# Optimization experiments

Measured on AMD Instinct MI355X. Metric: run time of the kernel, lower is better.

The kernel has to match this reference:

```python
import jax, jax.numpy as jnp
import numpy as np

N_HEAD = 16
D_MODEL = 1024
D_HEAD = 64
B = 2
S = 2048      # query length
M = 512       # memory length
K = S + M     # key length
L = 2 * K - 1 # relative position table length
SCALE = 1.0 / np.sqrt(D_MODEL)  # NOTE: module scales by 1/sqrt(d_model), not d_head
EPS = 1e-5


def layer_norm(x, gamma, beta):
    mu = jnp.mean(x, axis=-1, keepdims=True)
    var = jnp.mean(jnp.square(x - mu), axis=-1, keepdims=True)
    return (x - mu) * jax.lax.rsqrt(var + EPS) * gamma + beta


def skew(qpos, mem_len):
    # qpos: (B, H, S, 2K-1) -> relative-position scores aligned to keys (B, H, S, K)
    b, h, s, l = qpos.shape
    k_len = (l + 1) // 2
    pad = jnp.full((b, h, s, 1), -jnp.inf, dtype=qpos.dtype)
    rel = jnp.concatenate([qpos, pad], axis=-1)          # (B,H,S,2K)
    rel = rel.reshape(b, h, s * (l + 1))[..., : s * l]    # drop tail, shift rows
    rel = rel.reshape(b, h, s, l)
    start = (k_len - 1) - mem_len
    return rel[..., start : start + k_len]


def setup_inputs() -> dict:
    key = jax.random.key(0)
    ks = jax.random.split(key, 8)
    w_scale = 1.0 / np.sqrt(D_MODEL)
    hidden = jax.random.normal(ks[0], (B, S, D_MODEL), jnp.float32)
    memory = jax.random.normal(ks[1], (B, M, D_MODEL), jnp.float32)
    pos_emb = jax.random.normal(ks[2], (B, L, D_HEAD), jnp.float32)
    Wq = jax.random.normal(ks[3], (D_MODEL, N_HEAD * D_HEAD), jnp.float32) * w_scale
    Wk = jax.random.normal(ks[4], (D_MODEL, N_HEAD * D_HEAD), jnp.float32) * w_scale
    Wv = jax.random.normal(ks[5], (D_MODEL, N_HEAD * D_HEAD), jnp.float32) * w_scale
    Wo = jax.random.normal(ks[6], (N_HEAD * D_HEAD, D_MODEL), jnp.float32) * w_scale
    gamma = jnp.ones((D_MODEL,), jnp.float32)
    beta = jnp.zeros((D_MODEL,), jnp.float32)
    # causal mask with memory: query i may attend keys j <= i + M; True = drop
    i = jnp.arange(S)[:, None]
    j = jnp.arange(K)[None, :]
    mask = j > (i + M)  # (S, K) bool
    return {"hidden": hidden, "pos_emb": pos_emb, "memory": memory,
            "Wq": Wq, "Wk": Wk, "Wv": Wv, "Wo": Wo,
            "gamma": gamma, "beta": beta, "mask": mask}


def reference(hidden, pos_emb, memory, Wq, Wk, Wv, Wo, gamma, beta, mask):
    combined = jnp.concatenate([memory, hidden], axis=1)  # (B, K, D)
    hn = layer_norm(hidden, gamma, beta)                  # pre_lnorm
    cn = layer_norm(combined, gamma, beta)
    q = (hn @ Wq).reshape(B, S, N_HEAD, D_HEAD).transpose(0, 2, 1, 3)  # (B,H,S,Dh)
    k = (cn @ Wk).reshape(B, K, N_HEAD, D_HEAD).transpose(0, 2, 1, 3)  # (B,H,K,Dh)
    v = (cn @ Wv).reshape(B, K, N_HEAD, D_HEAD).transpose(0, 2, 1, 3)  # (B,H,K,Dh)
    scores = jnp.einsum("bhsd,bhkd->bhsk", q, k)           # content term
    qpos = jnp.einsum("bhsd,bld->bhsl", q, pos_emb)        # position term (B,H,S,2K-1)
    scores = (scores + skew(qpos, M)) * SCALE
    scores = jnp.where(mask[None, None], -jnp.inf, scores)
    attn = jax.nn.softmax(scores, axis=-1)
    atten_vec = jnp.einsum("bhsk,bhkd->bshd", attn, v).reshape(B, S, N_HEAD * D_HEAD)
    output = atten_vec @ Wo
    # faithful quirk: residual uses the layer-normed hidden when pre_lnorm=True
    return hn + output
```

## Files before the change

### kernel.cpp

```cpp
#include <hip/hip_runtime.h>

typedef unsigned short u16;
typedef float f32x4 __attribute__((ext_vector_type(4)));
typedef short short8 __attribute__((ext_vector_type(8)));

#define MFMA_BF16(a, b, c) __builtin_amdgcn_mfma_f32_16x16x32_bf16((a), (b), (c), 0, 0, 0)

#define NEG_BIG (-30000.0f)

typedef __attribute__((address_space(1))) const void gas_void;
typedef __attribute__((address_space(3))) void las_void;

__device__ __forceinline__ float bf2f(u16 v) {
  union { unsigned int u; float f; } c; c.u = ((unsigned int)v) << 16; return c.f;
}
__device__ __forceinline__ u16 f2bf(float f) {
  union { float f; unsigned int u; } c; c.f = f;
  return (u16)((c.u + 0x7fffu + ((c.u >> 16) & 1u)) >> 16);
}

__global__ __launch_bounds__(256) void cast_pe_k(const float* __restrict__ src, u16* __restrict__ dst,
                                                 int n4, int* __restrict__ ctr) {
  const int idx = blockIdx.x * 256 + threadIdx.x;
  if (idx == 0) *ctr = 0;
  if (idx >= n4) return;
  const float4 d = *(const float4*)&src[idx * 4];
  ushort4 o;
  o.x = f2bf(d.x); o.y = f2bf(d.y); o.z = f2bf(d.z); o.w = f2bf(d.w);
  *(ushort4*)&dst[idx * 4] = o;
}

__global__ __launch_bounds__(256) void transpose_k(const float* __restrict__ W0, const float* __restrict__ W1,
                                                   const float* __restrict__ W2, const float* __restrict__ W3,
                                                   u16* __restrict__ Wt) {
  __shared__ float t[32][33];
  const float* W = (blockIdx.z == 0) ? W0 : (blockIdx.z == 1) ? W1 : (blockIdx.z == 2) ? W2 : W3;
  u16* dst = Wt + (size_t)blockIdx.z * 1024 * 1024;
  const int tx = threadIdx.x, ty = threadIdx.y;
  const int x0 = blockIdx.x * 32, y0 = blockIdx.y * 32;
#pragma unroll
  for (int i = 0; i < 32; i += 8)
    t[ty + i][tx] = W[(size_t)(y0 + ty + i) * 1024 + x0 + tx];
  __syncthreads();
#pragma unroll
  for (int i = 0; i < 32; i += 8)
    dst[(size_t)(x0 + ty + i) * 1024 + y0 + tx] = f2bf(t[tx][ty + i]);
}

__global__ __launch_bounds__(256) void ln_k(const float* __restrict__ hid, const float* __restrict__ mem,
                                            const float* __restrict__ gam, const float* __restrict__ bet,
                                            u16* __restrict__ cn) {
  const int row = blockIdx.x;
  const int b = (row >= 2560) ? 1 : 0;
  const int r = row - b * 2560;
  const float* src = (r < 512) ? (mem + ((size_t)b * 512 + r) * 1024)
                               : (hid + ((size_t)b * 2048 + (r - 512)) * 1024);
  const int tid = threadIdx.x;
  const float4 d = *(const float4*)&src[tid * 4];
  float x[4] = {d.x, d.y, d.z, d.w};
  float s = x[0] + x[1] + x[2] + x[3];
  float q = x[0]*x[0] + x[1]*x[1] + x[2]*x[2] + x[3]*x[3];
#pragma unroll
  for (int o = 1; o < 64; o <<= 1) { s += __shfl_xor(s, o); q += __shfl_xor(q, o); }
  __shared__ float sb[4], qsb[4];
  const int wave = tid >> 6;
  if ((tid & 63) == 0) { sb[wave] = s; qsb[wave] = q; }
  __syncthreads();
  s = sb[0] + sb[1] + sb[2] + sb[3];
  q = qsb[0] + qsb[1] + qsb[2] + qsb[3];
  const float mu = s * (1.0f / 1024.0f);
  const float var = q * (1.0f / 1024.0f) - mu * mu;
  const float rstd = rsqrtf(fmaxf(var, 0.0f) + 1e-5f);
  u16 o4[4];
#pragma unroll
  for (int i = 0; i < 4; ++i) {
    const int c = tid * 4 + i;
    o4[i] = f2bf((x[i] - mu) * rstd * gam[c] + bet[c]);
  }
  uint2 pk;
  pk.x = (unsigned)o4[0] | ((unsigned)o4[1] << 16);
  pk.y = (unsigned)o4[2] | ((unsigned)o4[3] << 16);
  *(uint2*)&cn[((size_t)b * 2560 + r) * 1024 + tid * 4] = pk;
}

__global__ __launch_bounds__(256, 3) void gemm128_k(const u16* __restrict__ A, const u16* __restrict__ Bt,
                                                    u16* __restrict__ qb, u16* __restrict__ kbo,
                                                    u16* __restrict__ vtb) {
  __shared__ u16 smem[16384];
  const int tid = threadIdx.x;
  const int lane = tid & 63, w = tid >> 6;
  const int quad = lane >> 4, l15 = lane & 15, r7 = l15 & 7;
  const int wr = w >> 1, wc = w & 1;
  const int row0 = blockIdx.y * 128, col0 = blockIdx.x * 128;
  const int rloc = w * 8 + (lane >> 3);
  const int cg = ((lane & 7) ^ ((lane >> 3) & 7)) * 8;
  const u16* ga = A + (size_t)(row0 + rloc) * 1024 + cg;
  const u16* gb = Bt + (size_t)(col0 + rloc) * 1024 + cg;
  f32x4 z = {0.f, 0.f, 0.f, 0.f};
  f32x4 acc[4][4];
#pragma unroll
  for (int m = 0; m < 4; ++m)
#pragma unroll
    for (int n = 0; n < 4; ++n) acc[m][n] = z;
  for (int kt = 0; kt < 16; ++kt) {
    const int k0 = kt * 64;
#pragma unroll
    for (int g2 = 0; g2 < 4; ++g2) {
      __builtin_amdgcn_global_load_lds((gas_void*)(ga + (size_t)g2 * 32 * 1024 + k0),
                                       (las_void*)(smem + (g2 * 32 + w * 8) * 64), 16, 0, 0);
      __builtin_amdgcn_global_load_lds((gas_void*)(gb + (size_t)g2 * 32 * 1024 + k0),
                                       (las_void*)(smem + 8192 + (g2 * 32 + w * 8) * 64), 16, 0, 0);
    }
    __syncthreads();
    short8 af0[4], af1[4];
#pragma unroll
    for (int m = 0; m < 4; ++m) {
      const int row = wr * 64 + m * 16 + l15;
      af0[m] = *(const short8*)&smem[row * 64 + (quad ^ r7) * 8];
      af1[m] = *(const short8*)&smem[row * 64 + ((quad + 4) ^ r7) * 8];
    }
#pragma unroll
    for (int n = 0; n < 4; ++n) {
      const int row = wc * 64 + n * 16 + l15;
      const short8 bf0 = *(const short8*)&smem[8192 + row * 64 + (quad ^ r7) * 8];
      const short8 bf1 = *(const short8*)&smem[8192 + row * 64 + ((quad + 4) ^ r7) * 8];
#pragma unroll
      for (int m = 0; m < 4; ++m) {
        acc[m][n] = MFMA_BF16(af0[m], bf0, acc[m][n]);
        acc[m][n] = MFMA_BF16(af1[m], bf1, acc[m][n]);
      }
    }
    __syncthreads();
  }
  const int nc = col0 >> 10;
  if (nc != 2) {
#pragma unroll
    for (int m = 0; m < 4; ++m) {
#pragma unroll
      for (int n = 0; n < 4; ++n) {
#pragma unroll
        for (int r = 0; r < 4; ++r) {
          const int R = row0 + wr * 64 + m * 16 + quad * 4 + r;
          const int C = col0 + wc * 64 + n * 16 + l15;
          const float v = acc[m][n][r];
          const int c = C & 1023, h = c >> 6, dh = c & 63;
          const int b = (R >= 2560) ? 1 : 0, kk = R - b * 2560;
          if (nc == 0) {
            if (kk >= 512)
              qb[(((size_t)(b * 16 + h)) * 2048 + (kk - 512)) * 64 + dh] = f2bf(v * 0.03125f);
          } else {
            kbo[(((size_t)(b * 16 + h)) * 2560 + kk) * 64 + dh] = f2bf(v);
          }
        }
      }
    }
  } else {
#pragma unroll
    for (int m = 0; m < 4; ++m)
#pragma unroll
      for (int n = 0; n < 4; ++n)
#pragma unroll
        for (int r = 0; r < 4; ++r) {
          const int rl = wr * 64 + m * 16 + quad * 4 + r;
          const int cl = wc * 64 + n * 16 + l15;
          smem[cl * 128 + (rl ^ ((cl & 7) << 3))] = f2bf(acc[m][n][r]);
        }
    __syncthreads();
    const int bb = (row0 >= 2560) ? 1 : 0;
    const int kk0 = row0 - bb * 2560;
#pragma unroll
    for (int half = 0; half < 2; ++half) {
      const int cl = (tid >> 2) + half * 64;
      const int c = (col0 - 2048) + cl;
      const int hh = c >> 6, dh = c & 63;
      u16* dst = &vtb[(((size_t)(bb * 16 + hh)) * 64 + dh) * 2560 + kk0];
#pragma unroll
      for (int inner = 0; inner < 4; ++inner) {
        const int rl = inner * 32 + (tid & 3) * 8;
        *(short8*)(dst + rl) = *(const short8*)&smem[cl * 128 + (rl ^ ((cl & 7) << 3))];
      }
    }
  }
}

__global__ __launch_bounds__(256, 3) void gemm_out_k(const u16* __restrict__ A, const u16* __restrict__ Bt,
                                                     float* __restrict__ outf,
                                                     const u16* __restrict__ resid) {
  __shared__ u16 smem[16384];
  const int tid = threadIdx.x;
  const int lane = tid & 63, w = tid >> 6;
  const int quad = lane >> 4, l15 = lane & 15, r7 = l15 & 7;
  const int wr = w >> 1, wc = w & 1;
  const int row0 = blockIdx.y * 128, col0 = blockIdx.x * 128;
  const int rloc = w * 8 + (lane >> 3);
  const int cg = ((lane & 7) ^ ((lane >> 3) & 7)) * 8;
  const u16* ga = A + (size_t)(row0 + rloc) * 1024 + cg;
  const u16* gb = Bt + (size_t)(col0 + rloc) * 1024 + cg;
  f32x4 z = {0.f, 0.f, 0.f, 0.f};
  f32x4 acc[4][4];
#pragma unroll
  for (int m = 0; m < 4; ++m)
#pragma unroll
    for (int n = 0; n < 4; ++n) acc[m][n] = z;
  for (int kt = 0; kt < 16; ++kt) {
    const int k0 = kt * 64;
#pragma unroll
    for (int g2 = 0; g2 < 4; ++g2) {
      __builtin_amdgcn_global_load_lds((gas_void*)(ga + (size_t)g2 * 32 * 1024 + k0),
                                       (las_void*)(smem + (g2 * 32 + w * 8) * 64), 16, 0, 0);
      __builtin_amdgcn_global_load_lds((gas_void*)(gb + (size_t)g2 * 32 * 1024 + k0),
                                       (las_void*)(smem + 8192 + (g2 * 32 + w * 8) * 64), 16, 0, 0);
    }
    __syncthreads();
    short8 af0[4], af1[4];
#pragma unroll
    for (int m = 0; m < 4; ++m) {
      const int row = wr * 64 + m * 16 + l15;
      af0[m] = *(const short8*)&smem[row * 64 + (quad ^ r7) * 8];
      af1[m] = *(const short8*)&smem[row * 64 + ((quad + 4) ^ r7) * 8];
    }
#pragma unroll
    for (int n = 0; n < 4; ++n) {
      const int row = wc * 64 + n * 16 + l15;
      const short8 bf0 = *(const short8*)&smem[8192 + row * 64 + (quad ^ r7) * 8];
      const short8 bf1 = *(const short8*)&smem[8192 + row * 64 + ((quad + 4) ^ r7) * 8];
#pragma unroll
      for (int m = 0; m < 4; ++m) {
        acc[m][n] = MFMA_BF16(af0[m], bf0, acc[m][n]);
        acc[m][n] = MFMA_BF16(af1[m], bf1, acc[m][n]);
      }
    }
    __syncthreads();
  }
#pragma unroll
  for (int m = 0; m < 4; ++m) {
#pragma unroll
    for (int n = 0; n < 4; ++n) {
#pragma unroll
      for (int r = 0; r < 4; ++r) {
        const int R = row0 + wr * 64 + m * 16 + quad * 4 + r;
        const int C = col0 + wc * 64 + n * 16 + l15;
        const size_t rrow = (size_t)(R >> 11) * 2560 + 512 + (R & 2047);
        outf[(size_t)R * 1024 + C] = acc[m][n][r] + bf2f(resid[rrow * 1024 + C]);
      }
    }
  }
}

__global__ __launch_bounds__(512, 4) void attn_k(const u16* __restrict__ q, const u16* __restrict__ kb,
                                                 const u16* __restrict__ vt, const u16* __restrict__ pe,
                                                 u16* __restrict__ p0, u16* __restrict__ p1,
                                                 float* __restrict__ l0, float* __restrict__ l1,
                                                 int* __restrict__ ctr) {
  __shared__ u16 Kt[2][64][64];
  __shared__ u16 Vt[2][64][64];
  __shared__ u16 Pw[8][16][68];
  volatile int* mailbox = (volatile int*)&Pw[0][0][64];
  const int tid = threadIdx.x, lane = tid & 63, wave = tid >> 6;
  const int quad = lane >> 4, l15 = lane & 15, r7 = l15 & 7;
  const int srow = wave * 8 + (lane >> 3);
  const int sch8 = ((lane & 7) ^ ((lane >> 3) & 7)) * 8;
  const f32x4 z = {0.f, 0.f, 0.f, 0.f};
  for (;;) {
    if (tid == 0) *mailbox = atomicAdd(ctr, 1);
    __syncthreads();
    const int item = *mailbox;
    if (item >= 1024) return;
    const int qt = 15 - (item >> 6);
    const int bh = (item & 63) >> 1, half = item & 1;
    const int b = bh >> 4, h = bh & 15;
    const int qi0 = qt * 128 + wave * 16;
    const int nh = qt + 5;
    const int t0 = half * nh, t1 = t0 + nh;
    const u16* qrow = q + ((size_t)bh * 2048 + qi0 + l15) * 64 + quad * 8;
    const short8 aq0 = *(const short8*)qrow;
    const short8 aq1 = *(const short8*)(qrow + 32);
    const u16* kp = kb + ((size_t)bh * 2560 + srow) * 64 + sch8;
    const u16* vp = vt + ((size_t)bh * 64 + srow) * 2560 + sch8;
    const u16* pp = pe + ((long)b * 5119 - qi0 + 2032 + l15) * 64 + quad * 8 + (size_t)t0 * 4096;
    f32x4 acc[4];
#pragma unroll
    for (int i = 0; i < 4; ++i) acc[i] = z;
    float lrow[4] = {0.f, 0.f, 0.f, 0.f};
    const int jlast = qi0 + 527;
    __builtin_amdgcn_global_load_lds((gas_void*)(kp + (size_t)t0 * 4096),
                                     (las_void*)(&Kt[0][wave * 8][0]), 16, 0, 0);
    __builtin_amdgcn_global_load_lds((gas_void*)(vp + t0 * 64),
                                     (las_void*)(&Vt[0][wave * 8][0]), 16, 0, 0);
    __syncthreads();
    for (int jt = t0; jt < t1; ++jt) {
      const int j0 = jt * 64;
      const int cur = (jt - t0) & 1;
      const int jn = (jt + 1 < t1) ? (jt + 1) : jt;
      __builtin_amdgcn_global_load_lds((gas_void*)(kp + (size_t)jn * 4096),
                                       (las_void*)(&Kt[cur ^ 1][wave * 8][0]), 16, 0, 0);
      __builtin_amdgcn_global_load_lds((gas_void*)(vp + jn * 64),
                                       (las_void*)(&Vt[cur ^ 1][wave * 8][0]), 16, 0, 0);
      if (j0 <= jlast) {
        short8 pb[5], pb2[5];
#pragma unroll
        for (int g = 0; g < 5; ++g) {
          pb[g]  = *(const short8*)(pp + 1024 * g);
          pb2[g] = *(const short8*)(pp + 1024 * g + 32);
        }
        f32x4 sc[4];
#pragma unroll
        for (int s = 0; s < 4; ++s) {
          sc[s] = MFMA_BF16(aq0, *(const short8*)&Kt[cur][16 * s + l15][(quad ^ r7) * 8], z);
          sc[s] = MFMA_BF16(aq1, *(const short8*)&Kt[cur][16 * s + l15][((quad + 4) ^ r7) * 8], sc[s]);
        }
        f32x4 qp[5];
#pragma unroll
        for (int g = 0; g < 5; ++g) {
          qp[g] = MFMA_BF16(aq0, pb[g], z);
          qp[g] = MFMA_BF16(aq1, pb2[g], qp[g]);
        }
#pragma unroll
        for (int r = 0; r < 4; ++r) {
          const int di = quad * 4 + r;
          const int o = l15 - di + 15;
          const int src = quad * 16 + (o & 15);
          const float g0 = __shfl(qp[0][r], src);
          const float g1 = __shfl(qp[1][r], src);
          const float g2 = __shfl(qp[2][r], src);
          const float g3 = __shfl(qp[3][r], src);
          const float g4 = __shfl(qp[4][r], src);
          const bool lo = (o < 16);
          float s0 = sc[0][r] + (lo ? g0 : g1);
          float s1 = sc[1][r] + (lo ? g1 : g2);
          float s2 = sc[2][r] + (lo ? g2 : g3);
          float s3 = sc[3][r] + (lo ? g3 : g4);
          const int jlim = qi0 + di + 512 - j0 - l15;
          if (0 > jlim)  s0 = NEG_BIG;
          if (16 > jlim) s1 = NEG_BIG;
          if (32 > jlim) s2 = NEG_BIG;
          if (48 > jlim) s3 = NEG_BIG;
          const float p0v = __expf(s0);
          const float p1v = __expf(s1);
          const float p2v = __expf(s2);
          const float p3v = __expf(s3);
          lrow[r] += (p0v + p1v) + (p2v + p3v);
          Pw[wave][di][l15]      = f2bf(p0v);
          Pw[wave][di][16 + l15] = f2bf(p1v);
          Pw[wave][di][32 + l15] = f2bf(p2v);
          Pw[wave][di][48 + l15] = f2bf(p3v);
        }
        asm volatile("s_waitcnt lgkmcnt(0)" ::: "memory");
        const short8 pf0 = *(const short8*)&Pw[wave][l15][quad * 8];
        const short8 pf1 = *(const short8*)&Pw[wave][l15][32 + quad * 8];
#pragma unroll
        for (int n = 0; n < 4; ++n) {
          acc[n] = MFMA_BF16(pf0, *(const short8*)&Vt[cur][16 * n + l15][(quad ^ r7) * 8], acc[n]);
          acc[n] = MFMA_BF16(pf1, *(const short8*)&Vt[cur][16 * n + l15][((quad + 4) ^ r7) * 8], acc[n]);
        }
      }
      __syncthreads();
      pp += 4096;
    }
    u16* od = half ? p1 : p0;
    float* ol = half ? l1 : l0;
#pragma unroll
    for (int r = 0; r < 4; ++r) {
      float lsum = lrow[r];
#pragma unroll
      for (int o = 1; o < 16; o <<= 1) lsum += __shfl_xor(lsum, o);
      const int s = qi0 + quad * 4 + r;
      if (l15 == 0) ol[(size_t)bh * 2048 + s] = lsum;
#pragma unroll
      for (int n = 0; n < 4; ++n) {
        const int c = h * 64 + n * 16 + l15;
        od[((size_t)b * 2048 + s) * 1024 + c] = f2bf(acc[n][r]);
      }
    }
  }
}

__global__ __launch_bounds__(256) void combine_k(u16* __restrict__ av, const u16* __restrict__ p1,
                                                 const float* __restrict__ l0, const float* __restrict__ l1) {
  const int idx = blockIdx.x * 256 + threadIdx.x;
  const int base = idx * 4;
  const int row = base >> 10;
  const int col = base & 1023;
  const int b = row >> 11, s = row & 2047;
  const int h = col >> 6;
  const size_t li = ((size_t)(b * 16 + h)) * 2048 + s;
  const float inv = 1.0f / (l0[li] + l1[li]);
  const ushort4 a0 = *(const ushort4*)&av[(size_t)base];
  const ushort4 a1 = *(const ushort4*)&p1[(size_t)base];
  ushort4 o;
  o.x = f2bf((bf2f(a0.x) + bf2f(a1.x)) * inv);
  o.y = f2bf((bf2f(a0.y) + bf2f(a1.y)) * inv);
  o.z = f2bf((bf2f(a0.z) + bf2f(a1.z)) * inv);
  o.w = f2bf((bf2f(a0.w) + bf2f(a1.w)) * inv);
  *(ushort4*)&av[(size_t)base] = o;
}

extern "C" void kernel_launch(void* const* d_in, const int* in_sizes, int n_in,
                              void* d_out, int out_size, void* d_ws, size_t ws_size,
                              hipStream_t stream) {
  const float* hidden = (const float*)d_in[0];
  const float* pe     = (const float*)d_in[1];
  const float* memv   = (const float*)d_in[2];
  const float* Wq     = (const float*)d_in[3];
  const float* Wk     = (const float*)d_in[4];
  const float* Wv     = (const float*)d_in[5];
  const float* Wo     = (const float*)d_in[6];
  const float* gam    = (const float*)d_in[7];
  const float* bet    = (const float*)d_in[8];

  u16* ws  = (u16*)d_ws;
  u16* cn  = ws;
  u16* qb  = cn  + (size_t)5120 * 1024;
  u16* kb  = qb  + (size_t)4096 * 1024;
  u16* vt  = kb  + (size_t)5120 * 1024;
  u16* av  = vt  + (size_t)5120 * 1024;
  u16* wt  = av  + (size_t)4096 * 1024;
  u16* peb = wt  + (size_t)4 * 1024 * 1024;
  u16* p1  = peb + (size_t)2 * 5119 * 64;
  float* l0 = (float*)(p1 + (size_t)4096 * 1024);
  float* l1 = l0 + (size_t)32 * 2048;
  int* ctr  = (int*)(l1 + (size_t)32 * 2048);

  const int pe_n4 = (2 * 5119 * 64) / 4;
  cast_pe_k<<<(pe_n4 + 255) / 256, 256, 0, stream>>>(pe, peb, pe_n4, ctr);
  ln_k<<<5120, 256, 0, stream>>>(hidden, memv, gam, bet, cn);
  transpose_k<<<dim3(32, 32, 4), dim3(32, 8), 0, stream>>>(Wq, Wk, Wv, Wo, wt);
  gemm128_k<<<dim3(24, 40), 256, 0, stream>>>(cn, wt, qb, kb, vt);
  attn_k<<<768, 512, 0, stream>>>(qb, kb, vt, peb, av, p1, l0, l1, ctr);
  combine_k<<<4096, 256, 0, stream>>>(av, p1, l0, l1);
  gemm_out_k<<<dim3(8, 32), 256, 0, stream>>>(av, wt + (size_t)3 * 1024 * 1024,
                                              (float*)d_out, cn);
}
```

Baseline: 313.5 us.

## Fuse split-K attention combine into attn kernel via per-tile completion counters

Removes the separate combine_k kernel. Each attention work item now bumps an atomic counter for its (query tile, batch-head) pair. The second half to finish reads the partner's partial output and row-sum, then writes the normalized bf16 result directly from its registers. This saves a kernel launch and a full read/write pass over the partial buffers, at the cost of extra fences and atomics. Only one thread's atomic follows the threadfence before the block barrier, so there is a possible ordering race.

```diff
diff --git a/kernel.cpp b/kernel.cpp
--- a/kernel.cpp
+++ b/kernel.cpp
@@ -20,9 +20,10 @@
 }
 
 __global__ __launch_bounds__(256) void cast_pe_k(const float* __restrict__ src, u16* __restrict__ dst,
-                                                 int n4, int* __restrict__ ctr) {
+                                                 int n4, int* __restrict__ ctr, int* __restrict__ done) {
   const int idx = blockIdx.x * 256 + threadIdx.x;
   if (idx == 0) *ctr = 0;
+  if (idx < 512) done[idx] = 0;
   if (idx >= n4) return;
   const float4 d = *(const float4*)&src[idx * 4];
   ushort4 o;
@@ -251,7 +252,7 @@
                                                  const u16* __restrict__ vt, const u16* __restrict__ pe,
                                                  u16* __restrict__ p0, u16* __restrict__ p1,
                                                  float* __restrict__ l0, float* __restrict__ l1,
-                                                 int* __restrict__ ctr) {
+                                                 int* __restrict__ ctr, int* __restrict__ done) {
   __shared__ u16 Kt[2][64][64];
   __shared__ u16 Vt[2][64][64];
   __shared__ u16 Pw[8][16][68];
@@ -262,9 +263,9 @@
   const int sch8 = ((lane & 7) ^ ((lane >> 3) & 7)) * 8;
   const f32x4 z = {0.f, 0.f, 0.f, 0.f};
   for (;;) {
-    if (tid == 0) *mailbox = atomicAdd(ctr, 1);
-    __syncthreads();
-    const int item = *mailbox;
+    if (tid == 0) mailbox[0] = atomicAdd(ctr, 1);
+    __syncthreads();
+    const int item = mailbox[0];
     if (item >= 1024) return;
     const int qt = 15 - (item >> 6);
     const int bh = (item & 63) >> 1, half = item & 1;
@@ -359,11 +360,13 @@
     }
     u16* od = half ? p1 : p0;
     float* ol = half ? l1 : l0;
+    float lsums[4];
 #pragma unroll
     for (int r = 0; r < 4; ++r) {
       float lsum = lrow[r];
 #pragma unroll
       for (int o = 1; o < 16; o <<= 1) lsum += __shfl_xor(lsum, o);
+      lsums[r] = lsum;
       const int s = qi0 + quad * 4 + r;
       if (l15 == 0) ol[(size_t)bh * 2048 + s] = lsum;
 #pragma unroll
@@ -372,27 +375,26 @@
         od[((size_t)b * 2048 + s) * 1024 + c] = f2bf(acc[n][r]);
       }
     }
-  }
-}
-
-__global__ __launch_bounds__(256) void combine_k(u16* __restrict__ av, const u16* __restrict__ p1,
-                                                 const float* __restrict__ l0, const float* __restrict__ l1) {
-  const int idx = blockIdx.x * 256 + threadIdx.x;
-  const int base = idx * 4;
-  const int row = base >> 10;
-  const int col = base & 1023;
-  const int b = row >> 11, s = row & 2047;
-  const int h = col >> 6;
-  const size_t li = ((size_t)(b * 16 + h)) * 2048 + s;
-  const float inv = 1.0f / (l0[li] + l1[li]);
-  const ushort4 a0 = *(const ushort4*)&av[(size_t)base];
-  const ushort4 a1 = *(const ushort4*)&p1[(size_t)base];
-  ushort4 o;
-  o.x = f2bf((bf2f(a0.x) + bf2f(a1.x)) * inv);
-  o.y = f2bf((bf2f(a0.y) + bf2f(a1.y)) * inv);
-  o.z = f2bf((bf2f(a0.z) + bf2f(a1.z)) * inv);
-  o.w = f2bf((bf2f(a0.w) + bf2f(a1.w)) * inv);
-  *(ushort4*)&av[(size_t)base] = o;
+    __threadfence();
+    if (tid == 0) mailbox[1] = atomicAdd(&done[qt * 32 + bh], 1);
+    __syncthreads();
+    if (mailbox[1] == 1) {
+      __threadfence();
+      const u16* po = half ? p0 : p1;
+      const float* lo_ = half ? l0 : l1;
+#pragma unroll
+      for (int r = 0; r < 4; ++r) {
+        const int s = qi0 + quad * 4 + r;
+        const float inv = 1.0f / (lsums[r] + lo_[(size_t)bh * 2048 + s]);
+#pragma unroll
+        for (int n = 0; n < 4; ++n) {
+          const int c = h * 64 + n * 16 + l15;
+          const size_t ix = ((size_t)b * 2048 + s) * 1024 + c;
+          p0[ix] = f2bf((acc[n][r] + bf2f(po[ix])) * inv);
+        }
+      }
+    }
+  }
 }
 
 extern "C" void kernel_launch(void* const* d_in, const int* in_sizes, int n_in,
@@ -420,14 +422,14 @@
   float* l0 = (float*)(p1 + (size_t)4096 * 1024);
   float* l1 = l0 + (size_t)32 * 2048;
   int* ctr  = (int*)(l1 + (size_t)32 * 2048);
+  int* done = ctr + 1;
 
   const int pe_n4 = (2 * 5119 * 64) / 4;
-  cast_pe_k<<<(pe_n4 + 255) / 256, 256, 0, stream>>>(pe, peb, pe_n4, ctr);
+  cast_pe_k<<<(pe_n4 + 255) / 256, 256, 0, stream>>>(pe, peb, pe_n4, ctr, done);
   ln_k<<<5120, 256, 0, stream>>>(hidden, memv, gam, bet, cn);
   transpose_k<<<dim3(32, 32, 4), dim3(32, 8), 0, stream>>>(Wq, Wk, Wv, Wo, wt);
   gemm128_k<<<dim3(24, 40), 256, 0, stream>>>(cn, wt, qb, kb, vt);
-  attn_k<<<768, 512, 0, stream>>>(qb, kb, vt, peb, av, p1, l0, l1, ctr);
-  combine_k<<<4096, 256, 0, stream>>>(av, p1, l0, l1);
+  attn_k<<<768, 512, 0, stream>>>(qb, kb, vt, peb, av, p1, l0, l1, ctr, done);
   gemm_out_k<<<dim3(8, 32), 256, 0, stream>>>(av, wt + (size_t)3 * 1024 * 1024,
                                               (float*)d_out, cn);
 }
```

After: 693.5 us. 121% more time.
